# Kernel tuning notes

Hardware: AMD Instinct MI355X
Metric: run time of the kernel (lower is better)

The kernel has to match this reference:

```python
import jax, jax.numpy as jnp
import numpy as np

N_NODES = 100000
N_EDGES = 3200000
N_IN = 5
N_OUT = 16


def setup_inputs() -> dict:
    key = jax.random.key(0)
    k1, k2, k3, k4 = jax.random.split(key, 4)
    atom = jax.random.normal(k1, (N_NODES, N_IN), dtype=jnp.float32)
    edge_index = jax.random.randint(k2, (2, N_EDGES), 0, N_NODES, dtype=jnp.int64)
    # Linear(n_input=5, n_neural=16) parameters
    W = jax.random.normal(k3, (N_OUT, N_IN), dtype=jnp.float32) / np.sqrt(N_IN)
    b = jax.random.normal(k4, (N_OUT,), dtype=jnp.float32) * 0.01
    return {"atom": atom, "edge_index": edge_index, "W": W, "b": b}


def reference(atom, edge_index, W, b):
    n = atom.shape[0]
    # add_self_loops
    loops = jnp.arange(n, dtype=edge_index.dtype)
    row = jnp.concatenate([edge_index[0], loops])  # source nodes [E+N]
    col = jnp.concatenate([edge_index[1], loops])  # target nodes [E+N]
    # x = Linear(atom)
    x = atom @ W.T + b  # [N, n_out]
    # degree over target index (includes self loops -> deg >= 1)
    deg = jax.ops.segment_sum(jnp.ones_like(col, dtype=x.dtype), col, num_segments=n)
    dis = deg ** -0.5  # deg_inv_sqrt, finite since deg >= 1
    norm = dis[row] * dis[col]  # [E+N]
    # gather-scale-scatter: message = norm * x_j, aggr='add' at col
    msgs = norm[:, None] * x[row]  # [E+N, n_out]
    out = jax.ops.segment_sum(msgs, col, num_segments=n)  # [N, n_out]
    return jax.nn.relu(out)
```

## Files before the change

kernel.cpp:

```cpp
#include <hip/hip_runtime.h>

#define N_IN 5
#define N_OUT 16
#define NB 256
#define BN 400
#define CAP 14336
#define SCAP 13584
#define BIN_MAGIC 10737419ull

__device__ __forceinline__ int bin_of(int c) {
    return (int)(((unsigned long long)(unsigned)c * BIN_MAGIC) >> 32);
}

__global__ __launch_bounds__(1024) void partition_kernel(
        const int* __restrict__ row, const int* __restrict__ col,
        int e, int* __restrict__ eb, int* __restrict__ cursor) {
    __shared__ int sEdge[4096];
    __shared__ unsigned char sBinA[4096];
    __shared__ int hist[NB];
    __shared__ int sA[NB];
    __shared__ int sB[NB];
    __shared__ int gbase[NB];
    const int tid = threadIdx.x;
    const int e4 = e >> 2;
    const int i = blockIdx.x * 1024 + tid;
    const bool valid = i < e4;
    int rr[4], cc[4], bb[4], pr[4];
    if (valid) {
        int4 r4 = ((const int4*)row)[i];
        int4 c4 = ((const int4*)col)[i];
        rr[0] = r4.x; rr[1] = r4.y; rr[2] = r4.z; rr[3] = r4.w;
        cc[0] = c4.x; cc[1] = c4.y; cc[2] = c4.z; cc[3] = c4.w;
    }
    if (tid < NB) hist[tid] = 0;
    __syncthreads();
    if (valid) {
#pragma unroll
        for (int j = 0; j < 4; ++j) {
            bb[j] = bin_of(cc[j]);
            pr[j] = atomicAdd(&hist[bb[j]], 1);
        }
    }
    __syncthreads();
    if (tid < NB) sA[tid] = hist[tid];
    __syncthreads();
    int* src = sA; int* dst = sB;
#pragma unroll
    for (int off = 1; off < NB; off <<= 1) {
        if (tid < NB) {
            int v = src[tid];
            if (tid >= off) v += src[tid - off];
            dst[tid] = v;
        }
        __syncthreads();
        int* t = src; src = dst; dst = t;
    }
    if (tid < NB) {
        int h = hist[tid];
        gbase[tid] = h ? atomicAdd(&cursor[tid], h) : 0;
        dst[tid] = src[tid] - h;
    }
    __syncthreads();
    int* startA = dst;
    if (valid) {
#pragma unroll
        for (int j = 0; j < 4; ++j) {
            int slot = startA[bb[j]] + pr[j];
            sEdge[slot] = ((cc[j] - bb[j] * BN) << 17) | rr[j];
            sBinA[slot] = (unsigned char)bb[j];
        }
    }
    __syncthreads();
    const int tot = src[NB - 1];
    for (int s = tid; s < tot; s += 1024) {
        int b = sBinA[s];
        int pos = gbase[b] + (s - startA[b]);
        if (pos < CAP) eb[b * CAP + pos] = sEdge[s];
    }
    if (blockIdx.x == 0) {
        for (int k = (e4 << 2) + tid; k < e; k += 1024) {
            int c = col[k];
            int b = bin_of(c);
            int o = atomicAdd(&cursor[b], 1);
            if (o < CAP) eb[b * CAP + o] = ((c - b * BN) << 17) | row[k];
        }
    }
}

__global__ __launch_bounds__(1024) void deg_datom_kernel(
        const int* __restrict__ eb, const int* __restrict__ cursor,
        const float* __restrict__ atom,
        float4* __restrict__ datom8, int n) {
    __shared__ int hist[BN];
    int bin = blockIdx.x;
    if (threadIdx.x < BN) hist[threadIdx.x] = 0;
    __syncthreads();
    int s0 = bin * CAP;
    int cnt = min(max(cursor[bin], 0), CAP);
    const int4* ebv = (const int4*)(eb + s0);
    int cnt4 = cnt >> 2;
    for (int i = threadIdx.x; i < cnt4; i += 1024) {
        int4 v = ebv[i];
        atomicAdd(&hist[v.x >> 17], 1);
        atomicAdd(&hist[v.y >> 17], 1);
        atomicAdd(&hist[v.z >> 17], 1);
        atomicAdd(&hist[v.w >> 17], 1);
    }
    for (int i = (cnt4 << 2) + (int)threadIdx.x; i < cnt; i += 1024)
        atomicAdd(&hist[eb[s0 + i] >> 17], 1);
    __syncthreads();
    int l = threadIdx.x;
    if (l >= BN) return;
    int node = bin * BN + l;
    if (node >= n) return;
    float d = rsqrtf((float)(hist[l] + 1));
    const float* ap = atom + (size_t)node * N_IN;
    datom8[2 * node]     = make_float4(d * ap[0], d * ap[1], d * ap[2], d * ap[3]);
    datom8[2 * node + 1] = make_float4(d * ap[4], d, 0.0f, 0.0f);
}

__global__ __launch_bounds__(1024) void sort_gather_kernel(
        const int* __restrict__ eb, const int* __restrict__ cursor,
        const float4* __restrict__ datom8,
        const float* __restrict__ atom,
        const float* __restrict__ W, const float* __restrict__ bias,
        float* __restrict__ out, int n) {
    __shared__ int lds[16384];
    int* sebs = lds;
    int* hist = lds + SCAP;
    int* sA   = lds + SCAP + 400;
    int* sB   = lds + SCAP + 800;
    float* sAcc = (float*)(lds + SCAP + 400);
    const int bin = blockIdx.x;
    const int tid = threadIdx.x;
    if (tid < BN) hist[tid] = 0;
    __syncthreads();
    const int s0 = bin * CAP;
    const int cnt = min(max(cursor[bin], 0), SCAP);
    const int cnt4 = cnt >> 2;
    const int4* ebv = (const int4*)(eb + s0);

    int4 e0, e1, e2, e3, k0, k1, k2, k3;
    const bool v0 = tid          < cnt4;
    const bool v1 = tid + 1024   < cnt4;
    const bool v2 = tid + 2048   < cnt4;
    const bool v3 = tid + 3072   < cnt4;
    if (v0) { e0 = ebv[tid];
        k0.x = atomicAdd(&hist[e0.x >> 17], 1); k0.y = atomicAdd(&hist[e0.y >> 17], 1);
        k0.z = atomicAdd(&hist[e0.z >> 17], 1); k0.w = atomicAdd(&hist[e0.w >> 17], 1); }
    if (v1) { e1 = ebv[tid + 1024];
        k1.x = atomicAdd(&hist[e1.x >> 17], 1); k1.y = atomicAdd(&hist[e1.y >> 17], 1);
        k1.z = atomicAdd(&hist[e1.z >> 17], 1); k1.w = atomicAdd(&hist[e1.w >> 17], 1); }
    if (v2) { e2 = ebv[tid + 2048];
        k2.x = atomicAdd(&hist[e2.x >> 17], 1); k2.y = atomicAdd(&hist[e2.y >> 17], 1);
        k2.z = atomicAdd(&hist[e2.z >> 17], 1); k2.w = atomicAdd(&hist[e2.w >> 17], 1); }
    if (v3) { e3 = ebv[tid + 3072];
        k3.x = atomicAdd(&hist[e3.x >> 17], 1); k3.y = atomicAdd(&hist[e3.y >> 17], 1);
        k3.z = atomicAdd(&hist[e3.z >> 17], 1); k3.w = atomicAdd(&hist[e3.w >> 17], 1); }
    int tl = -1, tk = 0;
    if (tid < (cnt & 3)) {
        tl = eb[s0 + (cnt4 << 2) + tid];
        tk = atomicAdd(&hist[tl >> 17], 1);
    }
    __syncthreads();

    const int mydeg = (tid < BN) ? hist[tid] : 0;
    if (tid < BN) sA[tid] = mydeg;
    __syncthreads();
    int* src = sA; int* dst = sB;
#pragma unroll
    for (int off = 1; off < 512; off <<= 1) {
        if (tid < BN) {
            int v = src[tid];
            if (tid >= off) v += src[tid - off];
            dst[tid] = v;
        }
        __syncthreads();
        int* t = src; src = dst; dst = t;
    }
    if (tid < BN) hist[tid] = src[tid] - mydeg;
    __syncthreads();

    if (v0) {
        sebs[hist[e0.x >> 17] + k0.x] = e0.x;
        sebs[hist[e0.y >> 17] + k0.y] = e0.y;
        sebs[hist[e0.z >> 17] + k0.z] = e0.z;
        sebs[hist[e0.w >> 17] + k0.w] = e0.w;
    }
    if (v1) {
        sebs[hist[e1.x >> 17] + k1.x] = e1.x;
        sebs[hist[e1.y >> 17] + k1.y] = e1.y;
        sebs[hist[e1.z >> 17] + k1.z] = e1.z;
        sebs[hist[e1.w >> 17] + k1.w] = e1.w;
    }
    if (v2) {
        sebs[hist[e2.x >> 17] + k2.x] = e2.x;
        sebs[hist[e2.y >> 17] + k2.y] = e2.y;
        sebs[hist[e2.z >> 17] + k2.z] = e2.z;
        sebs[hist[e2.w >> 17] + k2.w] = e2.w;
    }
    if (v3) {
        sebs[hist[e3.x >> 17] + k3.x] = e3.x;
        sebs[hist[e3.y >> 17] + k3.y] = e3.y;
        sebs[hist[e3.z >> 17] + k3.z] = e3.z;
        sebs[hist[e3.w >> 17] + k3.w] = e3.w;
    }
    if (tl >= 0) sebs[hist[tl >> 17] + tk] = tl;
    for (int q = tid; q < 6 * BN; q += 1024) sAcc[q] = 0.0f;
    __syncthreads();

    const int ept = (cnt + 1023) >> 10;
    int beg = tid * ept; if (beg > cnt) beg = cnt;
    int end = beg + ept; if (end > cnt) end = cnt;
    float a0 = 0.f, a1 = 0.f, a2 = 0.f, a3 = 0.f, a4 = 0.f, a5 = 0.f;
    int cur = -1;
    for (int ii = beg; ii < end; ++ii) {
        int v = sebs[ii];
        int l = v >> 17;
        if (l != cur) {
            if (cur >= 0) {
                atomicAdd(&sAcc[cur * 6 + 0], a0);
                atomicAdd(&sAcc[cur * 6 + 1], a1);
                atomicAdd(&sAcc[cur * 6 + 2], a2);
                atomicAdd(&sAcc[cur * 6 + 3], a3);
                atomicAdd(&sAcc[cur * 6 + 4], a4);
                atomicAdd(&sAcc[cur * 6 + 5], a5);
            }
            cur = l;
            a0 = a1 = a2 = a3 = a4 = a5 = 0.f;
        }
        int r = v & 0x1FFFF;
        float4 qa = datom8[2 * r];
        float4 qb = datom8[2 * r + 1];
        a0 += qa.x; a1 += qa.y; a2 += qa.z;
        a3 += qa.w; a4 += qb.x; a5 += qb.y;
    }
    if (cur >= 0) {
        atomicAdd(&sAcc[cur * 6 + 0], a0);
        atomicAdd(&sAcc[cur * 6 + 1], a1);
        atomicAdd(&sAcc[cur * 6 + 2], a2);
        atomicAdd(&sAcc[cur * 6 + 3], a3);
        atomicAdd(&sAcc[cur * 6 + 4], a4);
        atomicAdd(&sAcc[cur * 6 + 5], a5);
    }
    __syncthreads();

    if (tid >= BN) return;
    const int node = bin * BN + tid;
    if (node >= n) return;
    const float d = rsqrtf((float)(mydeg + 1));
    const float* ap = atom + (size_t)node * N_IN;
    float t5[5];
    t5[0] = d * (sAcc[tid * 6 + 0] + d * ap[0]);
    t5[1] = d * (sAcc[tid * 6 + 1] + d * ap[1]);
    t5[2] = d * (sAcc[tid * 6 + 2] + d * ap[2]);
    t5[3] = d * (sAcc[tid * 6 + 3] + d * ap[3]);
    t5[4] = d * (sAcc[tid * 6 + 4] + d * ap[4]);
    const float t1 = d * (sAcc[tid * 6 + 5] + d);
    float ov[N_OUT];
#pragma unroll
    for (int o = 0; o < N_OUT; ++o) {
        float a = bias[o] * t1;
#pragma unroll
        for (int k = 0; k < 5; ++k) a = fmaf(W[o * N_IN + k], t5[k], a);
        ov[o] = fmaxf(a, 0.0f);
    }
    float4* op = (float4*)(out + (size_t)node * N_OUT);
#pragma unroll
    for (int q = 0; q < 4; ++q)
        op[q] = make_float4(ov[4 * q], ov[4 * q + 1], ov[4 * q + 2], ov[4 * q + 3]);
}

extern "C" void kernel_launch(void* const* d_in, const int* in_sizes, int n_in,
                              void* d_out, int out_size, void* d_ws, size_t ws_size,
                              hipStream_t stream) {
    const float* atom = (const float*)d_in[0];
    const int*   eidx = (const int*)d_in[1];
    const float* W    = (const float*)d_in[2];
    const float* b    = (const float*)d_in[3];
    float* out = (float*)d_out;

    int n = in_sizes[0] / N_IN;
    int e = in_sizes[1] / 2;
    const int* row = eidx;
    const int* col = eidx + e;

    auto align256 = [](size_t v) { return (v + 255) & ~(size_t)255; };
    char* w = (char*)d_ws;
    int*    cursor = (int*)w;     w += align256(NB * 4);
    int*    eb     = (int*)w;     w += align256((size_t)NB * CAP * 4);
    float4* datom8 = (float4*)w;

    int nchunk = ((e >> 2) + 1023) / 1024;
    if (nchunk < 1) nchunk = 1;

    hipMemsetAsync(cursor, 0, NB * sizeof(int), stream);
    partition_kernel<<<nchunk, 1024, 0, stream>>>(row, col, e, eb, cursor);
    deg_datom_kernel<<<NB, 1024, 0, stream>>>(eb, cursor, atom, datom8, n);
    sort_gather_kernel<<<NB, 1024, 0, stream>>>(eb, cursor, datom8, atom, W, b, out, n);
}
```

Baseline: 132.3 us.

## Move per-bin counting sort into the degree kernel and write sorted edges back

Result: no change. 134.1 us (+1.4%).

```diff
diff --git a/kernel.cpp b/kernel.cpp
--- a/kernel.cpp
+++ b/kernel.cpp
@@ -87,50 +87,15 @@
     }
 }
 
-__global__ __launch_bounds__(1024) void deg_datom_kernel(
-        const int* __restrict__ eb, const int* __restrict__ cursor,
+__global__ __launch_bounds__(1024) void sort_quant_kernel(
+        int* __restrict__ eb, const int* __restrict__ cursor,
         const float* __restrict__ atom,
         float4* __restrict__ datom8, int n) {
-    __shared__ int hist[BN];
-    int bin = blockIdx.x;
-    if (threadIdx.x < BN) hist[threadIdx.x] = 0;
-    __syncthreads();
-    int s0 = bin * CAP;
-    int cnt = min(max(cursor[bin], 0), CAP);
-    const int4* ebv = (const int4*)(eb + s0);
-    int cnt4 = cnt >> 2;
-    for (int i = threadIdx.x; i < cnt4; i += 1024) {
-        int4 v = ebv[i];
-        atomicAdd(&hist[v.x >> 17], 1);
-        atomicAdd(&hist[v.y >> 17], 1);
-        atomicAdd(&hist[v.z >> 17], 1);
-        atomicAdd(&hist[v.w >> 17], 1);
-    }
-    for (int i = (cnt4 << 2) + (int)threadIdx.x; i < cnt; i += 1024)
-        atomicAdd(&hist[eb[s0 + i] >> 17], 1);
-    __syncthreads();
-    int l = threadIdx.x;
-    if (l >= BN) return;
-    int node = bin * BN + l;
-    if (node >= n) return;
-    float d = rsqrtf((float)(hist[l] + 1));
-    const float* ap = atom + (size_t)node * N_IN;
-    datom8[2 * node]     = make_float4(d * ap[0], d * ap[1], d * ap[2], d * ap[3]);
-    datom8[2 * node + 1] = make_float4(d * ap[4], d, 0.0f, 0.0f);
-}
-
-__global__ __launch_bounds__(1024) void sort_gather_kernel(
-        const int* __restrict__ eb, const int* __restrict__ cursor,
-        const float4* __restrict__ datom8,
-        const float* __restrict__ atom,
-        const float* __restrict__ W, const float* __restrict__ bias,
-        float* __restrict__ out, int n) {
-    __shared__ int lds[16384];
+    __shared__ __align__(16) int lds[SCAP + 4 + 1200];
     int* sebs = lds;
-    int* hist = lds + SCAP;
-    int* sA   = lds + SCAP + 400;
-    int* sB   = lds + SCAP + 800;
-    float* sAcc = (float*)(lds + SCAP + 400);
+    int* hist = lds + SCAP + 4;
+    int* sA   = lds + SCAP + 404;
+    int* sB   = lds + SCAP + 804;
     const int bin = blockIdx.x;
     const int tid = threadIdx.x;
     if (tid < BN) hist[tid] = 0;
@@ -206,6 +171,39 @@
         sebs[hist[e3.w >> 17] + k3.w] = e3.w;
     }
     if (tl >= 0) sebs[hist[tl >> 17] + tk] = tl;
+    if (tid < 4) sebs[cnt + tid] = 0;
+    __syncthreads();
+
+    int cntw = (cnt + 3) >> 2;
+    int4* ebw = (int4*)(eb + s0);
+    for (int s = tid; s < cntw; s += 1024)
+        ebw[s] = make_int4(sebs[4 * s], sebs[4 * s + 1],
+                           sebs[4 * s + 2], sebs[4 * s + 3]);
+
+    if (tid >= BN) return;
+    const int node = bin * BN + tid;
+    if (node >= n) return;
+    float d = rsqrtf((float)(mydeg + 1));
+    const float* ap = atom + (size_t)node * N_IN;
+    datom8[2 * node]     = make_float4(d * ap[0], d * ap[1], d * ap[2], d * ap[3]);
+    datom8[2 * node + 1] = make_float4(d * ap[4], d, 0.0f, 0.0f);
+}
+
+__global__ __launch_bounds__(1024) void gather_kernel(
+        const int* __restrict__ eb, const int* __restrict__ cursor,
+        const float4* __restrict__ datom8,
+        const float* __restrict__ W, const float* __restrict__ bias,
+        float* __restrict__ out, int n) {
+    __shared__ __align__(16) int sebs[SCAP];
+    __shared__ float sAcc[6 * BN];
+    const int bin = blockIdx.x;
+    const int tid = threadIdx.x;
+    const int s0 = bin * CAP;
+    const int cnt = min(max(cursor[bin], 0), SCAP);
+    const int cnt4 = cnt >> 2;
+    const int4* ebv = (const int4*)(eb + s0);
+    for (int i = tid; i < cnt4; i += 1024) ((int4*)sebs)[i] = ebv[i];
+    for (int i = (cnt4 << 2) + tid; i < cnt; i += 1024) sebs[i] = eb[s0 + i];
     for (int q = tid; q < 6 * BN; q += 1024) sAcc[q] = 0.0f;
     __syncthreads();
 
@@ -248,14 +246,15 @@
     if (tid >= BN) return;
     const int node = bin * BN + tid;
     if (node >= n) return;
-    const float d = rsqrtf((float)(mydeg + 1));
-    const float* ap = atom + (size_t)node * N_IN;
+    float4 qa = datom8[2 * node];
+    float4 qb = datom8[2 * node + 1];
+    const float d = qb.y;
     float t5[5];
-    t5[0] = d * (sAcc[tid * 6 + 0] + d * ap[0]);
-    t5[1] = d * (sAcc[tid * 6 + 1] + d * ap[1]);
-    t5[2] = d * (sAcc[tid * 6 + 2] + d * ap[2]);
-    t5[3] = d * (sAcc[tid * 6 + 3] + d * ap[3]);
-    t5[4] = d * (sAcc[tid * 6 + 4] + d * ap[4]);
+    t5[0] = d * (sAcc[tid * 6 + 0] + qa.x);
+    t5[1] = d * (sAcc[tid * 6 + 1] + qa.y);
+    t5[2] = d * (sAcc[tid * 6 + 2] + qa.z);
+    t5[3] = d * (sAcc[tid * 6 + 3] + qa.w);
+    t5[4] = d * (sAcc[tid * 6 + 4] + qb.x);
     const float t1 = d * (sAcc[tid * 6 + 5] + d);
     float ov[N_OUT];
 #pragma unroll
@@ -296,6 +295,6 @@
 
     hipMemsetAsync(cursor, 0, NB * sizeof(int), stream);
     partition_kernel<<<nchunk, 1024, 0, stream>>>(row, col, e, eb, cursor);
-    deg_datom_kernel<<<NB, 1024, 0, stream>>>(eb, cursor, atom, datom8, n);
-    sort_gather_kernel<<<NB, 1024, 0, stream>>>(eb, cursor, datom8, atom, W, b, out, n);
-}
+    sort_quant_kernel<<<NB, 1024, 0, stream>>>(eb, cursor, atom, datom8, n);
+    gather_kernel<<<NB, 1024, 0, stream>>>(eb, cursor, datom8, W, b, out, n);
+}
```
